# Kernel optimization log

Hardware: AMD Instinct MI355X
Metric: run time of the kernel (lower is better)

## Reference

```python
import jax, jax.numpy as jnp
import numpy as np

B = 4096
D_IN = 2048
D_H = 2048
W_SCALE = 0.02  # keep exp() gate pre-activations small / numerically safe


def setup_inputs() -> dict:
    key = jax.random.key(0)
    ks = jax.random.split(key, 16)
    inp = {
        "x": jax.random.normal(ks[0], (B, D_IN), jnp.float32),
        "h_prev": jax.random.normal(ks[1], (B, D_H), jnp.float32),
        "c_prev": jax.random.normal(ks[2], (B, D_H), jnp.float32),
        "n_prev": jax.random.uniform(ks[3], (B, D_H), jnp.float32),
    }
    # input->hidden weights (stored [in, out]; torch Linear computes x @ W.T + b,
    # equivalent to x @ W_here + b) and biases
    for i, name in enumerate(["i", "f", "o", "z"]):
        inp[f"W_{name}"] = jax.random.normal(ks[4 + i], (D_IN, D_H), jnp.float32) * W_SCALE
        inp[f"b_{name}"] = jax.random.normal(ks[8 + i], (D_H,), jnp.float32) * W_SCALE
        inp[f"U_{name}"] = jax.random.normal(ks[12 + i], (D_H, D_H), jnp.float32) * W_SCALE
    return inp


def reference(x, h_prev, c_prev, n_prev,
              W_i, b_i, U_i, W_f, b_f, U_f,
              W_o, b_o, U_o, W_z, b_z, U_z):
    # Gate pre-activations: 8 GEMMs fused pairwise per gate
    i = jnp.exp(x @ W_i + b_i + h_prev @ U_i)
    f = jnp.exp(x @ W_f + b_f + h_prev @ U_f)
    o = jax.nn.sigmoid(x @ W_o + b_o + h_prev @ U_o)
    z = jnp.tanh(x @ W_z + b_z + h_prev @ U_z)
    c = f * c_prev + i * z
    n = f * n_prev + i
    h = o * (c / (n + 1e-6))
    return (h, c, n)
```

## Files before the change

kernel.cpp:

```cpp
#include <hip/hip_runtime.h>
#include <hip/hip_bf16.h>
#include <stdint.h>

#define B_DIM 4096
#define DH    2048
#define K_DIM 4096
#define N_DIM 8192
#define NT    128

typedef __bf16  bf16x8 __attribute__((ext_vector_type(8)));
typedef float   f32x4  __attribute__((ext_vector_type(4)));

__device__ __forceinline__ unsigned short f2bf(float f) {
  unsigned int u = __float_as_uint(f);
  u += 0x7FFFu + ((u >> 16) & 1u);
  return (unsigned short)(u >> 16);
}

__global__ void cast_cat_A(const float* __restrict__ x, const float* __restrict__ h,
                           unsigned short* __restrict__ Abuf) {
  int idx = blockIdx.x * 256 + threadIdx.x;
  const int half = B_DIM * (DH / 4);
  bool isx = (idx < half);
  int i2 = isx ? idx : idx - half;
  int b  = i2 >> 9;
  int c4 = i2 & 511;
  const float* src = (isx ? x : h) + (((size_t)b) << 11) + (c4 << 2);
  float4 v = *(const float4*)src;
  ushort4 o;
  o.x = f2bf(v.x); o.y = f2bf(v.y); o.z = f2bf(v.z); o.w = f2bf(v.w);
  int col = (isx ? 0 : DH) + (c4 << 2);
  *(ushort4*)(Abuf + (size_t)b * K_DIM + col) = o;
}

__global__ void transpose_cast_B(const float* __restrict__ Wi, const float* __restrict__ Ui,
                                 const float* __restrict__ Wf, const float* __restrict__ Uf,
                                 const float* __restrict__ Wo, const float* __restrict__ Uo,
                                 const float* __restrict__ Wz, const float* __restrict__ Uz,
                                 unsigned short* __restrict__ Bt) {
  __shared__ unsigned short lds[64 * 68];
  const int k0 = blockIdx.x * 64;
  const int g  = blockIdx.y >> 5;
  const int j0 = (blockIdx.y & 31) * 64;
  const float* W = (g == 0) ? Wi : (g == 1) ? Wf : (g == 2) ? Wo : Wz;
  const float* U = (g == 0) ? Ui : (g == 1) ? Uf : (g == 2) ? Uo : Uz;
  const float* src = ((k0 < DH) ? (W + (size_t)k0 * DH)
                                : (U + (size_t)(k0 - DH) * DH)) + j0;
  const int t  = threadIdx.x;
  const int tk = t >> 4;
  const int tj = t & 15;
  float4 v[4];
  #pragma unroll
  for (int r = 0; r < 4; ++r)
    v[r] = *(const float4*)(src + (size_t)(tk * 4 + r) * DH + tj * 4);
  #pragma unroll
  for (int jq = 0; jq < 4; ++jq) {
    int n = tj * 4 + jq;
    ushort4 w;
    w.x = f2bf(((const float*)&v[0])[jq]);
    w.y = f2bf(((const float*)&v[1])[jq]);
    w.z = f2bf(((const float*)&v[2])[jq]);
    w.w = f2bf(((const float*)&v[3])[jq]);
    *(ushort4*)(lds + n * 68 + tk * 4) = w;
  }
  __syncthreads();
  #pragma unroll
  for (int r = 0; r < 4; ++r) {
    int slot = r * 256 + t;
    int nn = slot >> 4;
    int c8 = slot & 15;
    int j  = j0 + nn;
    int np = ((j >> 5) << 7) + ((j & 16) << 2) + (g << 4) + (j & 15);
    *(ushort4*)(Bt + (size_t)np * K_DIM + k0 + (c8 << 2)) =
        *(const ushort4*)(lds + nn * 68 + (c8 << 2));
  }
}

__global__ __launch_bounds__(512, 2) void gemm_gates(const unsigned short* __restrict__ A,
                                                     const unsigned short* __restrict__ Bt,
                                                     const float* __restrict__ bi, const float* __restrict__ bf,
                                                     const float* __restrict__ bo, const float* __restrict__ bz,
                                                     const float* __restrict__ cprev, const float* __restrict__ nprev,
                                                     float* __restrict__ out) {
  __shared__ alignas(16) unsigned short lds[65536];
  unsigned short* As = lds;
  unsigned short* Bs = lds + 32768;

  const int t    = threadIdx.x;
  const int w    = t >> 6;
  const int lane = t & 63;
  const int lm   = lane & 15;
  const int kg   = lane >> 4;
  const int wm   = w >> 2;
  const int wn   = w & 3;

  const int flat = blockIdx.y * 32 + blockIdx.x;
  const int swzb = (flat & 7) * 64 + (flat >> 3);
  const int bx   = swzb & 31;
  const int by   = swzb >> 5;
  const int m0   = by * 256;
  const int n0   = bx * 256;

  const int r4 = lane >> 2, c4 = lane & 3;
  const int rowS0 = w * 32 + r4;
  const int rowS1 = rowS0 + 16;
  const int kby0 = (c4 * 16) ^ (((rowS0 >> 1) & 3) << 4);
  const int kby1 = (c4 * 16) ^ (((rowS1 >> 1) & 3) << 4);
  const unsigned short* pa0 = A  + (size_t)(m0 + rowS0) * K_DIM + (kby0 >> 1);
  const unsigned short* pa1 = A  + (size_t)(m0 + rowS1) * K_DIM + (kby1 >> 1);
  const unsigned short* pb0 = Bt + (size_t)(n0 + rowS0) * K_DIM + (kby0 >> 1);
  const unsigned short* pb1 = Bt + (size_t)(n0 + rowS1) * K_DIM + (kby1 >> 1);
  const int ldsQ0 = (w * 32) * 32;
  const int ldsQ1 = (w * 32 + 16) * 32;

  const int aoff = (wm * 128 + lm) * 64 + ((kg * 16) ^ (((lm >> 1) & 3) << 4));
  const int boff = (wn * 64  + lm) * 64 + ((kg * 16) ^ (((lm >> 1) & 3) << 4));
  const char* Asc = (const char*)As;
  const char* Bsc = (const char*)Bs;

  f32x4 acc[8][4] = {};

#define STAGE_A(tile) do {                                                                            \
    const int _buf = (tile) & 3;                                                                      \
    const size_t _k = (size_t)(tile) * 32;                                                            \
    __builtin_amdgcn_global_load_lds((const __attribute__((address_space(1))) unsigned int*)(pa0 + _k), \
        (__attribute__((address_space(3))) unsigned int*)(As + _buf * 8192 + ldsQ0), 16, 0, 0);       \
    __builtin_amdgcn_global_load_lds((const __attribute__((address_space(1))) unsigned int*)(pa1 + _k), \
        (__attribute__((address_space(3))) unsigned int*)(As + _buf * 8192 + ldsQ1), 16, 0, 0);       \
  } while (0)
#define STAGE_B(tile) do {                                                                            \
    const int _buf = (tile) & 3;                                                                      \
    const size_t _k = (size_t)(tile) * 32;                                                            \
    __builtin_amdgcn_global_load_lds((const __attribute__((address_space(1))) unsigned int*)(pb0 + _k), \
        (__attribute__((address_space(3))) unsigned int*)(Bs + _buf * 8192 + ldsQ0), 16, 0, 0);       \
    __builtin_amdgcn_global_load_lds((const __attribute__((address_space(1))) unsigned int*)(pb1 + _k), \
        (__attribute__((address_space(3))) unsigned int*)(Bs + _buf * 8192 + ldsQ1), 16, 0, 0);       \
  } while (0)

  STAGE_A(0); STAGE_B(0); STAGE_A(1); STAGE_B(1); STAGE_A(2); STAGE_B(2);
  asm volatile("s_waitcnt vmcnt(8)" ::: "memory");
  __builtin_amdgcn_s_barrier();
  asm volatile("" ::: "memory");

  for (int kt = 0; kt < NT; ++kt) {
    const int cur = kt & 3;
    const char* ab = Asc + cur * 16384 + aoff;
    const char* bb = Bsc + cur * 16384 + boff;
    bf16x8 av[4], bv[4];

    #pragma unroll
    for (int ni = 0; ni < 4; ++ni) bv[ni] = *(const bf16x8*)(bb + ni * 1024);
    #pragma unroll
    for (int i = 0; i < 4; ++i) av[i] = *(const bf16x8*)(ab + i * 1024);
    if (kt + 3 < NT) STAGE_A(kt + 3);
    __builtin_amdgcn_s_barrier();
    asm volatile("s_waitcnt lgkmcnt(0)" ::: "memory");
    __builtin_amdgcn_s_setprio(1);
    #pragma unroll
    for (int i = 0; i < 4; ++i)
      #pragma unroll
      for (int ni = 0; ni < 4; ++ni)
        acc[i][ni] = __builtin_amdgcn_mfma_f32_16x16x32_bf16(av[i], bv[ni], acc[i][ni], 0, 0, 0);
    __builtin_amdgcn_s_setprio(0);
    __builtin_amdgcn_s_barrier();
    asm volatile("" ::: "memory");

    #pragma unroll
    for (int i = 0; i < 4; ++i) av[i] = *(const bf16x8*)(ab + 4096 + i * 1024);
    if (kt + 3 < NT) STAGE_B(kt + 3);
    __builtin_amdgcn_s_barrier();
    asm volatile("s_waitcnt lgkmcnt(0)" ::: "memory");
    __builtin_amdgcn_s_setprio(1);
    #pragma unroll
    for (int i = 0; i < 4; ++i)
      #pragma unroll
      for (int ni = 0; ni < 4; ++ni)
        acc[4 + i][ni] = __builtin_amdgcn_mfma_f32_16x16x32_bf16(av[i], bv[ni], acc[4 + i][ni], 0, 0, 0);
    __builtin_amdgcn_s_setprio(0);
    if (kt + 3 < NT)      asm volatile("s_waitcnt vmcnt(8)" ::: "memory");
    else if (kt + 2 < NT) asm volatile("s_waitcnt vmcnt(4)" ::: "memory");
    else                  asm volatile("s_waitcnt vmcnt(0)" ::: "memory");
    __builtin_amdgcn_s_barrier();
    asm volatile("" ::: "memory");
  }

  const int jj = bx * 64 + (wn >> 1) * 32 + (wn & 1) * 16 + lm;
  const float vbi = bi[jj], vbf = bf[jj], vbo = bo[jj], vbz = bz[jj];
  #pragma unroll
  for (int mi = 0; mi < 8; ++mi) {
    const int mrow = m0 + wm * 128 + mi * 16 + kg * 4;
    #pragma unroll
    for (int r = 0; r < 4; ++r) {
      const size_t idx = (size_t)(mrow + r) * DH + jj;
      float pi = acc[mi][0][r] + vbi;
      float pf = acc[mi][1][r] + vbf;
      float po = acc[mi][2][r] + vbo;
      float pz = acc[mi][3][r] + vbz;
      float iv = __expf(pi);
      float fv = __expf(pf);
      float ov = 1.0f / (1.0f + __expf(-po));
      float t2 = __expf(2.0f * pz);
      float zv = 1.0f - 2.0f / (t2 + 1.0f);
      float cv = fv * cprev[idx] + iv * zv;
      float nv = fv * nprev[idx] + iv;
      out[idx]            = ov * (cv / (nv + 1e-6f));
      out[8388608 + idx]  = cv;
      out[16777216 + idx] = nv;
    }
  }
#undef STAGE_A
#undef STAGE_B
}

extern "C" void kernel_launch(void* const* d_in, const int* in_sizes, int n_in,
                              void* d_out, int out_size, void* d_ws, size_t ws_size,
                              hipStream_t stream) {
  const float* x      = (const float*)d_in[0];
  const float* h_prev = (const float*)d_in[1];
  const float* c_prev = (const float*)d_in[2];
  const float* n_prev = (const float*)d_in[3];
  const float* W_i = (const float*)d_in[4];  const float* b_i = (const float*)d_in[5];  const float* U_i = (const float*)d_in[6];
  const float* W_f = (const float*)d_in[7];  const float* b_f = (const float*)d_in[8];  const float* U_f = (const float*)d_in[9];
  const float* W_o = (const float*)d_in[10]; const float* b_o = (const float*)d_in[11]; const float* U_o = (const float*)d_in[12];
  const float* W_z = (const float*)d_in[13]; const float* b_z = (const float*)d_in[14]; const float* U_z = (const float*)d_in[15];
  float* out = (float*)d_out;

  char* ws = (char*)d_ws;
  unsigned short* Abuf = (unsigned short*)ws;
  unsigned short* Bt   = (unsigned short*)(ws + 33554432);

  cast_cat_A<<<16384, 256, 0, stream>>>(x, h_prev, Abuf);
  transpose_cast_B<<<dim3(64, 128), 256, 0, stream>>>(W_i, U_i, W_f, U_f, W_o, U_o, W_z, U_z, Bt);
  gemm_gates<<<dim3(32, 16), 512, 0, stream>>>(Abuf, Bt, b_i, b_f, b_o, b_z, c_prev, n_prev, out);
}
```

Before: 571.6 us.

## Drop intra-iteration barriers and stagger wave half-tile compute order

Removes the two mid-iteration workgroup barriers in the GEMM main loop. Waves are split into two groups by a wave-uniform flag: one group computes the A-upper half-tile first and the other the lower half first. The aim is to spread LDS reads and MFMA bursts across waves instead of lockstepping them, which should reduce barrier stalls and LDS contention. The cost is a duplicated, larger loop body and reliance on the single end-of-iteration barrier, plus compiler-inserted waits, for buffer safety.

```diff
diff --git a/kernel.cpp b/kernel.cpp
--- a/kernel.cpp
+++ b/kernel.cpp
@@ -93,6 +93,7 @@
   const int kg   = lane >> 4;
   const int wm   = w >> 2;
   const int wn   = w & 3;
+  const int stag = (w ^ (w >> 2)) & 1;
 
   const int flat = blockIdx.y * 32 + blockIdx.x;
   const int swzb = (flat & 7) * 64 + (flat >> 3);
@@ -150,33 +151,51 @@
 
     #pragma unroll
     for (int ni = 0; ni < 4; ++ni) bv[ni] = *(const bf16x8*)(bb + ni * 1024);
-    #pragma unroll
-    for (int i = 0; i < 4; ++i) av[i] = *(const bf16x8*)(ab + i * 1024);
-    if (kt + 3 < NT) STAGE_A(kt + 3);
-    __builtin_amdgcn_s_barrier();
-    asm volatile("s_waitcnt lgkmcnt(0)" ::: "memory");
-    __builtin_amdgcn_s_setprio(1);
-    #pragma unroll
-    for (int i = 0; i < 4; ++i)
-      #pragma unroll
-      for (int ni = 0; ni < 4; ++ni)
-        acc[i][ni] = __builtin_amdgcn_mfma_f32_16x16x32_bf16(av[i], bv[ni], acc[i][ni], 0, 0, 0);
-    __builtin_amdgcn_s_setprio(0);
-    __builtin_amdgcn_s_barrier();
-    asm volatile("" ::: "memory");
-
-    #pragma unroll
-    for (int i = 0; i < 4; ++i) av[i] = *(const bf16x8*)(ab + 4096 + i * 1024);
-    if (kt + 3 < NT) STAGE_B(kt + 3);
-    __builtin_amdgcn_s_barrier();
-    asm volatile("s_waitcnt lgkmcnt(0)" ::: "memory");
-    __builtin_amdgcn_s_setprio(1);
-    #pragma unroll
-    for (int i = 0; i < 4; ++i)
-      #pragma unroll
-      for (int ni = 0; ni < 4; ++ni)
-        acc[4 + i][ni] = __builtin_amdgcn_mfma_f32_16x16x32_bf16(av[i], bv[ni], acc[4 + i][ni], 0, 0, 0);
-    __builtin_amdgcn_s_setprio(0);
+
+    if (stag == 0) {
+      #pragma unroll
+      for (int i = 0; i < 4; ++i) av[i] = *(const bf16x8*)(ab + i * 1024);
+      if (kt + 3 < NT) STAGE_A(kt + 3);
+      __builtin_amdgcn_s_setprio(1);
+      #pragma unroll
+      for (int i = 0; i < 4; ++i)
+        #pragma unroll
+        for (int ni = 0; ni < 4; ++ni)
+          acc[i][ni] = __builtin_amdgcn_mfma_f32_16x16x32_bf16(av[i], bv[ni], acc[i][ni], 0, 0, 0);
+      __builtin_amdgcn_s_setprio(0);
+      #pragma unroll
+      for (int i = 0; i < 4; ++i) av[i] = *(const bf16x8*)(ab + 4096 + i * 1024);
+      if (kt + 3 < NT) STAGE_B(kt + 3);
+      __builtin_amdgcn_s_setprio(1);
+      #pragma unroll
+      for (int i = 0; i < 4; ++i)
+        #pragma unroll
+        for (int ni = 0; ni < 4; ++ni)
+          acc[4 + i][ni] = __builtin_amdgcn_mfma_f32_16x16x32_bf16(av[i], bv[ni], acc[4 + i][ni], 0, 0, 0);
+      __builtin_amdgcn_s_setprio(0);
+    } else {
+      #pragma unroll
+      for (int i = 0; i < 4; ++i) av[i] = *(const bf16x8*)(ab + 4096 + i * 1024);
+      if (kt + 3 < NT) STAGE_A(kt + 3);
+      __builtin_amdgcn_s_setprio(1);
+      #pragma unroll
+      for (int i = 0; i < 4; ++i)
+        #pragma unroll
+        for (int ni = 0; ni < 4; ++ni)
+          acc[4 + i][ni] = __builtin_amdgcn_mfma_f32_16x16x32_bf16(av[i], bv[ni], acc[4 + i][ni], 0, 0, 0);
+      __builtin_amdgcn_s_setprio(0);
+      #pragma unroll
+      for (int i = 0; i < 4; ++i) av[i] = *(const bf16x8*)(ab + i * 1024);
+      if (kt + 3 < NT) STAGE_B(kt + 3);
+      __builtin_amdgcn_s_setprio(1);
+      #pragma unroll
+      for (int i = 0; i < 4; ++i)
+        #pragma unroll
+        for (int ni = 0; ni < 4; ++ni)
+          acc[i][ni] = __builtin_amdgcn_mfma_f32_16x16x32_bf16(av[i], bv[ni], acc[i][ni], 0, 0, 0);
+      __builtin_amdgcn_s_setprio(0);
+    }
+
     if (kt + 3 < NT)      asm volatile("s_waitcnt vmcnt(8)" ::: "memory");
     else if (kt + 2 < NT) asm volatile("s_waitcnt vmcnt(4)" ::: "memory");
     else                  asm volatile("s_waitcnt vmcnt(0)" ::: "memory");
```

Measured after the change: 576.7 us. No clear change (+0.9%).

## Shrink GEMM block tile to 128x256 with 4 waves and triple buffering

Applied to the files above, without the earlier changes.

The block tile drops from 256x256 with 8 waves to 128x256 with 4 waves, and the grid grows to 1024 blocks. LDS buffering goes from four stages to three, and each K step now issues one combined stage of A and B loads instead of two half-steps with separate barriers. Each wave computes a 64x128 sub-tile, interleaving A-fragment LDS reads with MFMA groups. This cuts LDS use and barriers per K step, which may allow more blocks per CU, at the cost of lower arithmetic intensity per block and more global traffic for B.

```diff
diff --git a/kernel.cpp b/kernel.cpp
--- a/kernel.cpp
+++ b/kernel.cpp
@@ -76,140 +76,134 @@
   }
 }
 
-__global__ __launch_bounds__(512, 2) void gemm_gates(const unsigned short* __restrict__ A,
+__global__ __launch_bounds__(256, 2) void gemm_gates(const unsigned short* __restrict__ A,
                                                      const unsigned short* __restrict__ Bt,
                                                      const float* __restrict__ bi, const float* __restrict__ bf,
                                                      const float* __restrict__ bo, const float* __restrict__ bz,
                                                      const float* __restrict__ cprev, const float* __restrict__ nprev,
                                                      float* __restrict__ out) {
-  __shared__ alignas(16) unsigned short lds[65536];
+  __shared__ alignas(16) unsigned short lds[36864];
   unsigned short* As = lds;
-  unsigned short* Bs = lds + 32768;
+  unsigned short* Bs = lds + 12288;
 
   const int t    = threadIdx.x;
   const int w    = t >> 6;
   const int lane = t & 63;
   const int lm   = lane & 15;
   const int kg   = lane >> 4;
-  const int wm   = w >> 2;
-  const int wn   = w & 3;
+  const int wm2  = w >> 1;
+  const int wn2  = w & 1;
 
   const int flat = blockIdx.y * 32 + blockIdx.x;
-  const int swzb = (flat & 7) * 64 + (flat >> 3);
+  const int swzb = (flat & 7) * 128 + (flat >> 3);
   const int bx   = swzb & 31;
   const int by   = swzb >> 5;
-  const int m0   = by * 256;
+  const int m0   = by * 128;
   const int n0   = bx * 256;
 
-  const int r4 = lane >> 2, c4 = lane & 3;
-  const int rowS0 = w * 32 + r4;
-  const int rowS1 = rowS0 + 16;
-  const int kby0 = (c4 * 16) ^ (((rowS0 >> 1) & 3) << 4);
-  const int kby1 = (c4 * 16) ^ (((rowS1 >> 1) & 3) << 4);
-  const unsigned short* pa0 = A  + (size_t)(m0 + rowS0) * K_DIM + (kby0 >> 1);
-  const unsigned short* pa1 = A  + (size_t)(m0 + rowS1) * K_DIM + (kby1 >> 1);
-  const unsigned short* pb0 = Bt + (size_t)(n0 + rowS0) * K_DIM + (kby0 >> 1);
-  const unsigned short* pb1 = Bt + (size_t)(n0 + rowS1) * K_DIM + (kby1 >> 1);
-  const int ldsQ0 = (w * 32) * 32;
-  const int ldsQ1 = (w * 32 + 16) * 32;
-
-  const int aoff = (wm * 128 + lm) * 64 + ((kg * 16) ^ (((lm >> 1) & 3) << 4));
-  const int boff = (wn * 64  + lm) * 64 + ((kg * 16) ^ (((lm >> 1) & 3) << 4));
+  const int rowA = t >> 2;
+  const int kby  = ((t & 3) << 4) ^ (((t >> 3) & 3) << 4);
+  const unsigned short* pa0 = A  + (size_t)(m0 + rowA) * K_DIM + (kby >> 1);
+  const unsigned short* pa1 = pa0 + (size_t)64  * K_DIM;
+  const unsigned short* pb0 = Bt + (size_t)(n0 + rowA) * K_DIM + (kby >> 1);
+  const unsigned short* pb1 = pb0 + (size_t)64  * K_DIM;
+  const unsigned short* pb2 = pb0 + (size_t)128 * K_DIM;
+  const unsigned short* pb3 = pb0 + (size_t)192 * K_DIM;
+  const int ldsA0 = w * 512;
+  const int ldsA1 = 2048 + w * 512;
+  const int ldsB0 = w * 512;
+  const int ldsB1 = 2048 + w * 512;
+  const int ldsB2 = 4096 + w * 512;
+  const int ldsB3 = 6144 + w * 512;
+
+  const int aoff = (wm2 * 64  + lm) * 64 + ((kg * 16) ^ (((lm >> 1) & 3) << 4));
+  const int boff = (wn2 * 128 + lm) * 64 + ((kg * 16) ^ (((lm >> 1) & 3) << 4));
   const char* Asc = (const char*)As;
   const char* Bsc = (const char*)Bs;
 
-  f32x4 acc[8][4] = {};
-
-#define STAGE_A(tile) do {                                                                            \
-    const int _buf = (tile) & 3;                                                                      \
-    const size_t _k = (size_t)(tile) * 32;                                                            \
-    __builtin_amdgcn_global_load_lds((const __attribute__((address_space(1))) unsigned int*)(pa0 + _k), \
-        (__attribute__((address_space(3))) unsigned int*)(As + _buf * 8192 + ldsQ0), 16, 0, 0);       \
-    __builtin_amdgcn_global_load_lds((const __attribute__((address_space(1))) unsigned int*)(pa1 + _k), \
-        (__attribute__((address_space(3))) unsigned int*)(As + _buf * 8192 + ldsQ1), 16, 0, 0);       \
+  f32x4 acc[4][8] = {};
+
+#define GLL(src, dst) __builtin_amdgcn_global_load_lds( \
+    (const __attribute__((address_space(1))) unsigned int*)(src), \
+    (__attribute__((address_space(3))) unsigned int*)(dst), 16, 0, 0)
+#define STAGE(tile, buf) do {                                   \
+    const size_t _k = (size_t)(tile) * 32;                      \
+    GLL(pa0 + _k, As + (buf) * 4096 + ldsA0);                   \
+    GLL(pa1 + _k, As + (buf) * 4096 + ldsA1);                   \
+    GLL(pb0 + _k, Bs + (buf) * 8192 + ldsB0);                   \
+    GLL(pb1 + _k, Bs + (buf) * 8192 + ldsB1);                   \
+    GLL(pb2 + _k, Bs + (buf) * 8192 + ldsB2);                   \
+    GLL(pb3 + _k, Bs + (buf) * 8192 + ldsB3);                   \
   } while (0)
-#define STAGE_B(tile) do {                                                                            \
-    const int _buf = (tile) & 3;                                                                      \
-    const size_t _k = (size_t)(tile) * 32;                                                            \
-    __builtin_amdgcn_global_load_lds((const __attribute__((address_space(1))) unsigned int*)(pb0 + _k), \
-        (__attribute__((address_space(3))) unsigned int*)(Bs + _buf * 8192 + ldsQ0), 16, 0, 0);       \
-    __builtin_amdgcn_global_load_lds((const __attribute__((address_space(1))) unsigned int*)(pb1 + _k), \
-        (__attribute__((address_space(3))) unsigned int*)(Bs + _buf * 8192 + ldsQ1), 16, 0, 0);       \
-  } while (0)
-
-  STAGE_A(0); STAGE_B(0); STAGE_A(1); STAGE_B(1); STAGE_A(2); STAGE_B(2);
-  asm volatile("s_waitcnt vmcnt(8)" ::: "memory");
+
+  STAGE(0, 0); STAGE(1, 1);
+  asm volatile("s_waitcnt vmcnt(6)" ::: "memory");
   __builtin_amdgcn_s_barrier();
   asm volatile("" ::: "memory");
 
+  int cur = 0, stg = 2;
   for (int kt = 0; kt < NT; ++kt) {
-    const int cur = kt & 3;
-    const char* ab = Asc + cur * 16384 + aoff;
+    const char* ab = Asc + cur * 8192  + aoff;
     const char* bb = Bsc + cur * 16384 + boff;
-    bf16x8 av[4], bv[4];
+    bf16x8 bv[8], avA, avB;
 
     #pragma unroll
-    for (int ni = 0; ni < 4; ++ni) bv[ni] = *(const bf16x8*)(bb + ni * 1024);
-    #pragma unroll
-    for (int i = 0; i < 4; ++i) av[i] = *(const bf16x8*)(ab + i * 1024);
-    if (kt + 3 < NT) STAGE_A(kt + 3);
-    __builtin_amdgcn_s_barrier();
-    asm volatile("s_waitcnt lgkmcnt(0)" ::: "memory");
-    __builtin_amdgcn_s_setprio(1);
-    #pragma unroll
-    for (int i = 0; i < 4; ++i)
-      #pragma unroll
-      for (int ni = 0; ni < 4; ++ni)
-        acc[i][ni] = __builtin_amdgcn_mfma_f32_16x16x32_bf16(av[i], bv[ni], acc[i][ni], 0, 0, 0);
-    __builtin_amdgcn_s_setprio(0);
+    for (int ni = 0; ni < 8; ++ni) bv[ni] = *(const bf16x8*)(bb + ni * 1024);
+    avA = *(const bf16x8*)(ab);
+    if (kt + 2 < NT) STAGE(kt + 2, stg);
+
+#define MM(avr, mi) do {                                                                  \
+    __builtin_amdgcn_s_setprio(1);                                                        \
+    _Pragma("unroll")                                                                     \
+    for (int ni = 0; ni < 8; ++ni)                                                        \
+      acc[mi][ni] = __builtin_amdgcn_mfma_f32_16x16x32_bf16(avr, bv[ni], acc[mi][ni], 0, 0, 0); \
+    __builtin_amdgcn_s_setprio(0);                                                        \
+  } while (0)
+
+    avB = *(const bf16x8*)(ab + 1024);  MM(avA, 0);
+    avA = *(const bf16x8*)(ab + 2048);  MM(avB, 1);
+    avB = *(const bf16x8*)(ab + 3072);  MM(avA, 2);
+    MM(avB, 3);
+#undef MM
+
+    if (kt + 2 < NT) asm volatile("s_waitcnt vmcnt(6)" ::: "memory");
+    else             asm volatile("s_waitcnt vmcnt(0)" ::: "memory");
     __builtin_amdgcn_s_barrier();
     asm volatile("" ::: "memory");
-
+    cur = (cur == 2) ? 0 : cur + 1;
+    stg = (stg == 2) ? 0 : stg + 1;
+  }
+
+  const int jb = (bx * 2 + wn2) * 32;
+  #pragma unroll
+  for (int jh = 0; jh < 2; ++jh) {
+    const int j = jb + jh * 16 + lm;
+    const float vbi = bi[j], vbf = bf[j], vbo = bo[j], vbz = bz[j];
     #pragma unroll
-    for (int i = 0; i < 4; ++i) av[i] = *(const bf16x8*)(ab + 4096 + i * 1024);
-    if (kt + 3 < NT) STAGE_B(kt + 3);
-    __builtin_amdgcn_s_barrier();
-    asm volatile("s_waitcnt lgkmcnt(0)" ::: "memory");
-    __builtin_amdgcn_s_setprio(1);
-    #pragma unroll
-    for (int i = 0; i < 4; ++i)
+    for (int mi = 0; mi < 4; ++mi) {
+      const int mrow = m0 + wm2 * 64 + mi * 16 + kg * 4;
       #pragma unroll
-      for (int ni = 0; ni < 4; ++ni)
-        acc[4 + i][ni] = __builtin_amdgcn_mfma_f32_16x16x32_bf16(av[i], bv[ni], acc[4 + i][ni], 0, 0, 0);
-    __builtin_amdgcn_s_setprio(0);
-    if (kt + 3 < NT)      asm volatile("s_waitcnt vmcnt(8)" ::: "memory");
-    else if (kt + 2 < NT) asm volatile("s_waitcnt vmcnt(4)" ::: "memory");
-    else                  asm volatile("s_waitcnt vmcnt(0)" ::: "memory");
-    __builtin_amdgcn_s_barrier();
-    asm volatile("" ::: "memory");
-  }
-
-  const int jj = bx * 64 + (wn >> 1) * 32 + (wn & 1) * 16 + lm;
-  const float vbi = bi[jj], vbf = bf[jj], vbo = bo[jj], vbz = bz[jj];
-  #pragma unroll
-  for (int mi = 0; mi < 8; ++mi) {
-    const int mrow = m0 + wm * 128 + mi * 16 + kg * 4;
-    #pragma unroll
-    for (int r = 0; r < 4; ++r) {
-      const size_t idx = (size_t)(mrow + r) * DH + jj;
-      float pi = acc[mi][0][r] + vbi;
-      float pf = acc[mi][1][r] + vbf;
-      float po = acc[mi][2][r] + vbo;
-      float pz = acc[mi][3][r] + vbz;
-      float iv = __expf(pi);
-      float fv = __expf(pf);
-      float ov = 1.0f / (1.0f + __expf(-po));
-      float t2 = __expf(2.0f * pz);
-      float zv = 1.0f - 2.0f / (t2 + 1.0f);
-      float cv = fv * cprev[idx] + iv * zv;
-      float nv = fv * nprev[idx] + iv;
-      out[idx]            = ov * (cv / (nv + 1e-6f));
-      out[8388608 + idx]  = cv;
-      out[16777216 + idx] = nv;
+      for (int r = 0; r < 4; ++r) {
+        const size_t idx = (size_t)(mrow + r) * DH + j;
+        float pi = acc[mi][jh * 4 + 0][r] + vbi;
+        float pf = acc[mi][jh * 4 + 1][r] + vbf;
+        float po = acc[mi][jh * 4 + 2][r] + vbo;
+        float pz = acc[mi][jh * 4 + 3][r] + vbz;
+        float iv = __expf(pi);
+        float fv = __expf(pf);
+        float ov = 1.0f / (1.0f + __expf(-po));
+        float t2 = __expf(2.0f * pz);
+        float zv = 1.0f - 2.0f / (t2 + 1.0f);
+        float cv = fv * cprev[idx] + iv * zv;
+        float nv = fv * nprev[idx] + iv;
+        out[idx]            = ov * (cv / (nv + 1e-6f));
+        out[8388608 + idx]  = cv;
+        out[16777216 + idx] = nv;
+      }
     }
   }
-#undef STAGE_A
-#undef STAGE_B
+#undef STAGE
+#undef GLL
 }
 
 extern "C" void kernel_launch(void* const* d_in, const int* in_sizes, int n_in,
@@ -231,5 +225,5 @@
 
   cast_cat_A<<<16384, 256, 0, stream>>>(x, h_prev, Abuf);
   transpose_cast_B<<<dim3(64, 128), 256, 0, stream>>>(W_i, U_i, W_f, U_f, W_o, U_o, W_z, U_z, Bt);
-  gemm_gates<<<dim3(32, 16), 512, 0, stream>>>(Abuf, Bt, b_i, b_f, b_o, b_z, c_prev, n_prev, out);
-}
+  gemm_gates<<<dim3(32, 32), 256, 0, stream>>>(Abuf, Bt, b_i, b_f, b_o, b_z, c_prev, n_prev, out);
+}
```

Measured after the change: 666.9 us. +16.7%, slower.
